# Kernel tuning notes

Hardware: AMD Instinct MI355X
Metric: run time of the kernel (lower is better)

Reference implementation:

```python
import jax, jax.numpy as jnp
import numpy as np

N_ATOMS = 100000
N_EDGES = 400000
N_MOLS = 4000
D_ATOM = 64
D_MSG = 128
N_STEPS = 3
N_MSG_HID = 1
D_RO = 256
N_RO_HID = 2
D_OUT = 1


def setup_inputs() -> dict:
    key = jax.random.key(0)
    ks = jax.random.split(key, 20)

    def w(k, shape, fan_in):
        return jax.random.normal(k, shape, dtype=jnp.float32) / np.sqrt(fan_in)

    return {
        "atom_states": jax.random.normal(ks[0], (N_ATOMS, D_ATOM), dtype=jnp.float32),
        "edge_src": jax.random.randint(ks[1], (N_EDGES,), 0, N_ATOMS, dtype=jnp.int32),
        "edge_dst": jax.random.randint(ks[2], (N_EDGES,), 0, N_ATOMS, dtype=jnp.int32),
        "mol_ids": jnp.sort(jax.random.randint(ks[3], (N_ATOMS,), 0, N_MOLS, dtype=jnp.int32)),
        "ms_W_in": w(ks[4], (N_STEPS, 2 * D_ATOM, D_MSG), 2 * D_ATOM),
        "ms_b_in": w(ks[5], (N_STEPS, D_MSG), 2 * D_ATOM),
        "ms_W_h": w(ks[6], (N_STEPS, N_MSG_HID, D_MSG, D_MSG), D_MSG),
        "ms_b_h": w(ks[7], (N_STEPS, N_MSG_HID, D_MSG), D_MSG),
        "ms_W_out": w(ks[8], (N_STEPS, D_MSG, D_ATOM), D_MSG),
        "ms_b_out": w(ks[9], (N_STEPS, D_ATOM), D_MSG),
        "ro_W_in": w(ks[10], (D_ATOM, D_RO), D_ATOM),
        "ro_b_in": w(ks[11], (D_RO,), D_ATOM),
        "ro_W_h": w(ks[12], (N_RO_HID, D_RO, D_RO), D_RO),
        "ro_b_h": w(ks[13], (N_RO_HID, D_RO), D_RO),
        "ro_W_out": w(ks[14], (D_RO, D_OUT), D_RO),
        "ro_b_out": w(ks[15], (D_OUT,), D_RO),
    }


def reference(atom_states, edge_src, edge_dst, mol_ids,
              ms_W_in, ms_b_in, ms_W_h, ms_b_h, ms_W_out, ms_b_out,
              ro_W_in, ro_b_in, ro_W_h, ro_b_h, ro_W_out, ro_b_out):
    n_atoms = atom_states.shape[0]
    states = atom_states
    # Message passing: per edge, message = MLP_step(concat(state[src], state[dst]));
    # new atom state = sum of messages over the atom's edges (aggregated at src).
    for s in range(ms_W_in.shape[0]):
        msg = jnp.concatenate([states[edge_src], states[edge_dst]], axis=-1)  # [E, 2*D]
        h = jax.nn.relu(msg @ ms_W_in[s] + ms_b_in[s])                        # [E, D_MSG]
        for l in range(ms_W_h.shape[1]):
            h = jax.nn.relu(h @ ms_W_h[s, l] + ms_b_h[s, l])
        m = jax.nn.relu(h @ ms_W_out[s] + ms_b_out[s])                        # [E, D]
        states = jax.ops.segment_sum(m, edge_src, num_segments=n_atoms)       # [N, D]
    # Readout: molecule representation = sum of its atom states, then MLP.
    mol_repr = jax.ops.segment_sum(states, mol_ids, num_segments=N_MOLS)      # [M, D]
    out = jax.nn.relu(mol_repr @ ro_W_in + ro_b_in)
    for l in range(ro_W_h.shape[0]):
        out = jax.nn.relu(out @ ro_W_h[l] + ro_b_h[l])
    return out @ ro_W_out + ro_b_out                                          # [M, D_OUT]
```

## Files before the change

kernel.cpp:

```cpp
#include <hip/hip_runtime.h>
#include <hip/hip_bf16.h>

#define K_N_ATOMS 100000
#define K_N_EDGES 400000
#define K_N_MOLS  4000

typedef __attribute__((ext_vector_type(8))) short bf16x8;
typedef __attribute__((ext_vector_type(4))) float f32x4;

__device__ __forceinline__ unsigned short f2bf(float x) {
  union { __hip_bfloat16 b; unsigned short u; } c;
  c.b = __float2bfloat16(x);
  return c.u;
}

__device__ __forceinline__ float bf2f(unsigned short u) {
  union { float f; unsigned u; } c;
  c.u = ((unsigned)u) << 16;
  return c.f;
}

__device__ __forceinline__ unsigned pk2(float a, float b) {
  union { __hip_bfloat162 h; unsigned u; } c;
  c.h = __float22bfloat162_rn(make_float2(a, b));
  return c.u;
}

__device__ __forceinline__ bf16x8 pack8(float4 x, float4 y) {
  union { bf16x8 v; unsigned u[4]; } r;
  r.u[0] = pk2(x.x, x.y); r.u[1] = pk2(x.z, x.w);
  r.u[2] = pk2(y.x, y.y); r.u[3] = pk2(y.z, y.w);
  return r.v;
}

__device__ __forceinline__ float relu(float x) { return fmaxf(x, 0.f); }

__device__ __forceinline__ bf16x8 addrelu8(bf16x8 a, bf16x8 b) {
  union { bf16x8 v; unsigned short s[8]; } ua, ub;
  ua.v = a; ub.v = b;
  union { bf16x8 v; unsigned u[4]; } r;
#pragma unroll
  for (int q = 0; q < 4; ++q) {
    float x0 = relu(bf2f(ua.s[2 * q]) + bf2f(ub.s[2 * q]));
    float x1 = relu(bf2f(ua.s[2 * q + 1]) + bf2f(ub.s[2 * q + 1]));
    r.u[q] = pk2(x0, x1);
  }
  return r.v;
}

__global__ void prep_w(const float* __restrict__ Win, const float* __restrict__ Wh,
                       const float* __restrict__ Wout, unsigned short* __restrict__ wf) {
  int s = blockIdx.y;
  int flat = (blockIdx.x * 256 + threadIdx.x) * 4;
  if (flat < 16384) {
    const float* W = Win + s * 16384;
    unsigned short* dst = wf + s * 40960;
    int k = flat >> 7, j = flat & 127;
    float4 w4 = *(const float4*)(W + flat);
    float wv[4] = {w4.x, w4.y, w4.z, w4.w};
#pragma unroll
    for (int c = 0; c < 4; ++c) {
      int jj = j + c, kk = k;
      if (k >= 64) { kk = k - 64; jj += 128; }
      int jt = jj >> 4, ks = kk >> 5, ln = (jj & 15) + 16 * ((kk >> 3) & 3), i = kk & 7;
      dst[((jt * 2 + ks) * 64 + ln) * 8 + i] = f2bf(wv[c]);
    }
  } else if (flat < 32768) {
    const float* W = Wh + s * 16384;
    unsigned short* dst = wf + s * 40960 + 16384;
    int local = flat - 16384;
    int k = local >> 7, j = local & 127;
    float4 w4 = *(const float4*)(W + local);
    float wv[4] = {w4.x, w4.y, w4.z, w4.w};
    int ks = k >> 5, kr = (k >> 3) & 3, i = k & 7;
#pragma unroll
    for (int c = 0; c < 4; ++c) {
      int jj = j + c;
      int jt = jj >> 4, ln = (jj & 15) + 16 * kr;
      dst[((jt * 4 + ks) * 64 + ln) * 8 + i] = f2bf(wv[c]);
    }
  } else {
    const float* W = Wout + s * 8192;
    unsigned short* dst = wf + s * 40960 + 32768;
    int local = flat - 32768;
    int k = local >> 6, j = local & 63;
    float4 w4 = *(const float4*)(W + local);
    float wv[4] = {w4.x, w4.y, w4.z, w4.w};
    int ks = k >> 5, kr = (k >> 3) & 3, i = k & 7;
#pragma unroll
    for (int c = 0; c < 4; ++c) {
      int jj = j + c;
      int jt = jj >> 4, ln = (jj & 15) + 16 * kr;
      dst[((jt * 4 + ks) * 64 + ln) * 8 + i] = f2bf(wv[c]);
    }
  }
}

__global__ void k_hist(const int* __restrict__ esrc, int* __restrict__ cnt) {
  int t = blockIdx.x * 256 + threadIdx.x;
  if (t < K_N_EDGES) atomicAdd(&cnt[esrc[t]], 1);
}

__global__ void k_blocksum(const int* __restrict__ cnt, int* __restrict__ partial) {
  __shared__ int red[256];
  int i = blockIdx.x * 256 + threadIdx.x;
  red[threadIdx.x] = (i < K_N_ATOMS) ? cnt[i] : 0;
  __syncthreads();
  for (int off = 128; off; off >>= 1) {
    if (threadIdx.x < off) red[threadIdx.x] += red[threadIdx.x + off];
    __syncthreads();
  }
  if (!threadIdx.x) partial[blockIdx.x] = red[0];
}

__global__ void k_scanpart2(int* __restrict__ partial, int nb) {
  __shared__ int sh[512];
  int tid = threadIdx.x;
  int v = (tid < nb) ? partial[tid] : 0;
  sh[tid] = v;
  __syncthreads();
  for (int off = 1; off < 512; off <<= 1) {
    int t = (tid >= off) ? sh[tid - off] : 0;
    __syncthreads();
    sh[tid] += t;
    __syncthreads();
  }
  if (tid < nb) partial[tid] = sh[tid] - v;
}

__global__ void k_scanfinal(const int* __restrict__ cnt, const int* __restrict__ poffs,
                            int* __restrict__ start, int* __restrict__ cur) {
  __shared__ int sh[256];
  int tid = threadIdx.x;
  int i = blockIdx.x * 256 + tid;
  int v = (i < K_N_ATOMS) ? cnt[i] : 0;
  sh[tid] = v;
  __syncthreads();
  for (int off = 1; off < 256; off <<= 1) {
    int t = (tid >= off) ? sh[tid - off] : 0;
    __syncthreads();
    sh[tid] += t;
    __syncthreads();
  }
  int ex = sh[tid] - v + poffs[blockIdx.x];
  if (i < K_N_ATOMS) { start[i] = ex; cur[i] = ex; }
  if (i == K_N_ATOMS - 1) start[K_N_ATOMS] = ex + v;
}

__global__ void k_scatter(const int* __restrict__ esrc, const int* __restrict__ edst,
                          int* __restrict__ cur, int2* __restrict__ ep) {
  int t = blockIdx.x * 256 + threadIdx.x;
  if (t < K_N_EDGES) {
    int s = esrc[t];
    int p = atomicAdd(&cur[s], 1);
    ep[p] = make_int2(s, edst[t]);
  }
}

__global__ __launch_bounds__(256, 4) void fg_gemm0(
    const float* __restrict__ st_in, unsigned short* __restrict__ FG,
    const unsigned short* __restrict__ wfg, const float* __restrict__ bin) {
  const int tid = threadIdx.x;
  const int wave = tid >> 6, lane = tid & 63, lo = lane & 15, h = lane >> 4;
  const int atom0 = (blockIdx.x * 4 + wave) * 16;
  const int a = atom0 + lo;
  const int ac = (a < K_N_ATOMS) ? a : (K_N_ATOMS - 1);

  const float* row = st_in + (size_t)ac * 64 + h * 8;
  bf16x8 b0 = pack8(*(const float4*)row, *(const float4*)(row + 4));
  bf16x8 b1 = pack8(*(const float4*)(row + 32), *(const float4*)(row + 36));

#pragma unroll
  for (int jt = 0; jt < 16; ++jt) {
    f32x4 acc;
    if (jt < 8) acc = *(const f32x4*)(bin + jt * 16 + h * 4);
    else { acc[0] = 0.f; acc[1] = 0.f; acc[2] = 0.f; acc[3] = 0.f; }
    bf16x8 a0 = *(const bf16x8*)(wfg + ((jt * 2 + 0) * 64 + lane) * 8);
    bf16x8 a1 = *(const bf16x8*)(wfg + ((jt * 2 + 1) * 64 + lane) * 8);
    acc = __builtin_amdgcn_mfma_f32_16x16x32_bf16(a0, b0, acc, 0, 0, 0);
    acc = __builtin_amdgcn_mfma_f32_16x16x32_bf16(a1, b1, acc, 0, 0, 0);
    if (a < K_N_ATOMS)
      *(uint2*)(FG + (size_t)a * 256 + jt * 16 + h * 4) =
          make_uint2(pk2(acc[0], acc[1]), pk2(acc[2], acc[3]));
  }
}

__global__ __launch_bounds__(256, 4) void agg_fg(
    const unsigned short* __restrict__ m_buf, const int* __restrict__ start,
    unsigned short* __restrict__ FG,
    const unsigned short* __restrict__ wfg, const float* __restrict__ bin) {
  const int tid = threadIdx.x;
  const int wave = tid >> 6, lane = tid & 63, lo = lane & 15, h = lane >> 4;
  const int atom0 = (blockIdx.x * 4 + wave) * 16;
  const int a = atom0 + lo;

  int s = 0, e = 0;
  if (a < K_N_ATOMS) { s = start[a]; e = start[a + 1]; }

  float acc[16];
#pragma unroll
  for (int q = 0; q < 16; ++q) acc[q] = 0.f;
  for (int r = s; r < e; ++r) {
    const unsigned short* p = m_buf + (size_t)r * 64 + h * 8;
    union { bf16x8 v; unsigned short w[8]; } u0, u1;
    u0.v = *(const bf16x8*)(p);
    u1.v = *(const bf16x8*)(p + 32);
#pragma unroll
    for (int q = 0; q < 8; ++q) { acc[q] += bf2f(u0.w[q]); acc[8 + q] += bf2f(u1.w[q]); }
  }
  union { bf16x8 v; unsigned u[4]; } c0, c1;
#pragma unroll
  for (int q = 0; q < 4; ++q) {
    c0.u[q] = pk2(acc[2 * q], acc[2 * q + 1]);
    c1.u[q] = pk2(acc[8 + 2 * q], acc[8 + 2 * q + 1]);
  }
  bf16x8 b0 = c0.v, b1 = c1.v;

#pragma unroll
  for (int jt = 0; jt < 16; ++jt) {
    f32x4 d;
    if (jt < 8) d = *(const f32x4*)(bin + jt * 16 + h * 4);
    else { d[0] = 0.f; d[1] = 0.f; d[2] = 0.f; d[3] = 0.f; }
    bf16x8 a0 = *(const bf16x8*)(wfg + ((jt * 2 + 0) * 64 + lane) * 8);
    bf16x8 a1 = *(const bf16x8*)(wfg + ((jt * 2 + 1) * 64 + lane) * 8);
    d = __builtin_amdgcn_mfma_f32_16x16x32_bf16(a0, b0, d, 0, 0, 0);
    d = __builtin_amdgcn_mfma_f32_16x16x32_bf16(a1, b1, d, 0, 0, 0);
    if (a < K_N_ATOMS)
      *(uint2*)(FG + (size_t)a * 256 + jt * 16 + h * 4) =
          make_uint2(pk2(d[0], d[1]), pk2(d[2], d[3]));
  }
}

__device__ __forceinline__ void layer128_2(const unsigned short* wf,
                                           const float* __restrict__ bias,
                                           bf16x8 (&bfr)[2][4], unsigned (&p)[2][8][2],
                                           int lane, int h) {
#pragma unroll
  for (int jt = 0; jt < 8; ++jt) {
    f32x4 bv = *(const f32x4*)(bias + jt * 16 + h * 4);
    f32x4 a0 = bv, a1 = bv;
#pragma unroll
    for (int ks = 0; ks < 4; ++ks) {
      bf16x8 a = *(const bf16x8*)(wf + ((jt * 4 + ks) * 64 + lane) * 8);
      a0 = __builtin_amdgcn_mfma_f32_16x16x32_bf16(a, bfr[0][ks], a0, 0, 0, 0);
      a1 = __builtin_amdgcn_mfma_f32_16x16x32_bf16(a, bfr[1][ks], a1, 0, 0, 0);
    }
    p[0][jt][0] = pk2(relu(a0[0]), relu(a0[1])); p[0][jt][1] = pk2(relu(a0[2]), relu(a0[3]));
    p[1][jt][0] = pk2(relu(a1[0]), relu(a1[1])); p[1][jt][1] = pk2(relu(a1[2]), relu(a1[3]));
  }
}

__device__ __forceinline__ void transpose_p2(const unsigned (&p)[2][8][2], bf16x8 (&bfr)[2][4],
                                             int lo, int h) {
  const int hsel = (h & 1) * 2;
#pragma unroll
  for (int et = 0; et < 2; ++et) {
#pragma unroll
    for (int ks = 0; ks < 4; ++ks) {
      union { unsigned u[4]; bf16x8 v; } cv;
#pragma unroll
      for (int w = 0; w < 4; ++w) {
        int srcLane = lo + 16 * (hsel + (w >> 1));
        unsigned d0 = (unsigned)__shfl((int)p[et][2 * ks][w & 1], srcLane, 64);
        unsigned d1 = (unsigned)__shfl((int)p[et][2 * ks + 1][w & 1], srcLane, 64);
        cv.u[w] = (h < 2) ? d0 : d1;
      }
      bfr[et][ks] = cv.v;
    }
  }
}

__global__ __launch_bounds__(512, 4) void edge_msg4(
    const unsigned short* __restrict__ FG, unsigned short* __restrict__ m_buf,
    const int2* __restrict__ ep, const unsigned short* __restrict__ wf23,
    const float* __restrict__ b2, const float* __restrict__ b3) {
  __shared__ unsigned short wl[24576];
  const int tid = threadIdx.x;
  const int wave = tid >> 6, lane = tid & 63, lo = lane & 15, h = lane >> 4;
  const int ebase = blockIdx.x * 256 + wave * 32;

  int srcs[2], dsts[2];
  unsigned vmask = 0;
#pragma unroll
  for (int et = 0; et < 2; ++et) {
    int e = ebase + et * 16 + lo;
    if (e < K_N_EDGES) vmask |= 1u << et;
    int ec = (e < K_N_EDGES) ? e : (K_N_EDGES - 1);
    int2 pr = ep[ec];
    srcs[et] = pr.x;
    dsts[et] = pr.y;
  }

#pragma unroll
  for (int i = 0; i < 6; ++i)
    ((bf16x8*)wl)[i * 512 + tid] = ((const bf16x8*)wf23)[i * 512 + tid];
  __syncthreads();

  bf16x8 bfr[2][4];
#pragma unroll
  for (int et = 0; et < 2; ++et) {
    const unsigned short* pf = FG + (size_t)srcs[et] * 256 + h * 8;
    const unsigned short* pg = FG + (size_t)dsts[et] * 256 + 128 + h * 8;
#pragma unroll
    for (int ks = 0; ks < 4; ++ks) {
      bf16x8 f = *(const bf16x8*)(pf + ks * 32);
      bf16x8 g = *(const bf16x8*)(pg + ks * 32);
      bfr[et][ks] = addrelu8(f, g);
    }
  }

  unsigned p[2][8][2];
  layer128_2(wl, b2, bfr, p, lane, h);
  transpose_p2(p, bfr, lo, h);

  const unsigned short* w3 = wl + 16384;
#pragma unroll
  for (int jt = 0; jt < 4; ++jt) {
    f32x4 bv = *(const f32x4*)(b3 + jt * 16 + h * 4);
    f32x4 a0 = bv, a1 = bv;
#pragma unroll
    for (int ks = 0; ks < 4; ++ks) {
      bf16x8 a = *(const bf16x8*)(w3 + ((jt * 4 + ks) * 64 + lane) * 8);
      a0 = __builtin_amdgcn_mfma_f32_16x16x32_bf16(a, bfr[0][ks], a0, 0, 0, 0);
      a1 = __builtin_amdgcn_mfma_f32_16x16x32_bf16(a, bfr[1][ks], a1, 0, 0, 0);
    }
    f32x4 accs[2] = {a0, a1};
#pragma unroll
    for (int et = 0; et < 2; ++et) {
      if (vmask & (1u << et)) {
        int e = ebase + et * 16 + lo;
        *(uint2*)(m_buf + (size_t)e * 64 + jt * 16 + h * 4) =
            make_uint2(pk2(relu(accs[et][0]), relu(accs[et][1])),
                       pk2(relu(accs[et][2]), relu(accs[et][3])));
      }
    }
  }
}

__global__ __launch_bounds__(256) void seg_agg2(
    const unsigned short* __restrict__ m_buf, const int* __restrict__ start,
    unsigned short* __restrict__ stb_out) {
  int t = blockIdx.x * 256 + threadIdx.x;
  int a = t >> 3, sub = t & 7;
  if (a >= K_N_ATOMS) return;
  int s = start[a], e = start[a + 1];
  float acc[8] = {0.f, 0.f, 0.f, 0.f, 0.f, 0.f, 0.f, 0.f};
  for (int r = s; r < e; ++r) {
    union { bf16x8 v; unsigned short w[8]; } u;
    u.v = *(const bf16x8*)(m_buf + (size_t)r * 64 + sub * 8);
#pragma unroll
    for (int q = 0; q < 8; ++q) acc[q] += bf2f(u.w[q]);
  }
  union { bf16x8 v; unsigned u[4]; } r8;
#pragma unroll
  for (int q = 0; q < 4; ++q) r8.u[q] = pk2(acc[2 * q], acc[2 * q + 1]);
  *(bf16x8*)(stb_out + (size_t)a * 64 + sub * 8) = r8.v;
}

__global__ void mol_bounds(const int* __restrict__ mol_ids, int* __restrict__ start) {
  int a = blockIdx.x * 256 + threadIdx.x;
  if (a >= K_N_ATOMS) return;
  int id = mol_ids[a];
  int prev = (a == 0) ? -1 : mol_ids[a - 1];
  for (int m = prev + 1; m <= id; ++m) start[m] = a;
  if (a == K_N_ATOMS - 1)
    for (int m = id + 1; m <= K_N_MOLS; ++m) start[m] = K_N_ATOMS;
}

__global__ void mol_sum2(const unsigned short* __restrict__ stb, const int* __restrict__ start,
                         float* __restrict__ mol) {
  int t = blockIdx.x * 256 + threadIdx.x;
  int m = t >> 3, sub = t & 7;
  if (m >= K_N_MOLS) return;
  int s = start[m], e = start[m + 1];
  float acc[8] = {0.f, 0.f, 0.f, 0.f, 0.f, 0.f, 0.f, 0.f};
  for (int a = s; a < e; ++a) {
    union { bf16x8 v; unsigned short w[8]; } u;
    u.v = *(const bf16x8*)(stb + (size_t)a * 64 + sub * 8);
#pragma unroll
    for (int q = 0; q < 8; ++q) acc[q] += bf2f(u.w[q]);
  }
  float* p = mol + (size_t)m * 64 + sub * 8;
  *(float4*)(p) = make_float4(acc[0], acc[1], acc[2], acc[3]);
  *(float4*)(p + 4) = make_float4(acc[4], acc[5], acc[6], acc[7]);
}

template<int KDIM>
__global__ void mlp_layer8(const float* __restrict__ in, const float* __restrict__ W,
                           const float* __restrict__ bias, float* __restrict__ out) {
  __shared__ float in_l[8][KDIM + 4];
  int m0 = blockIdx.x * 8;
  int t = threadIdx.x;
  for (int flat = t; flat < 8 * KDIM; flat += 256) {
    int m = flat / KDIM, k = flat - m * KDIM;
    in_l[m][k] = in[(size_t)(m0 + m) * KDIM + k];
  }
  __syncthreads();
  int j = t;
  float b = bias[j];
  float acc[8];
#pragma unroll
  for (int m = 0; m < 8; ++m) acc[m] = b;
  for (int k = 0; k < KDIM; ++k) {
    float w = W[(size_t)k * 256 + j];
#pragma unroll
    for (int m = 0; m < 8; ++m) acc[m] += in_l[m][k] * w;
  }
#pragma unroll
  for (int m = 0; m < 8; ++m)
    out[(size_t)(m0 + m) * 256 + j] = fmaxf(acc[m], 0.f);
}

__global__ void mlp_out_k(const float* __restrict__ in, const float* __restrict__ W,
                          const float* __restrict__ bias, float* __restrict__ out) {
  int wave = threadIdx.x >> 6, lane = threadIdx.x & 63;
  int m = blockIdx.x * 4 + wave;
  if (m >= K_N_MOLS) return;
  float4 v = *(const float4*)(in + (size_t)m * 256 + lane * 4);
  float4 w = *(const float4*)(W + lane * 4);
  float s = v.x * w.x + v.y * w.y + v.z * w.z + v.w * w.w;
  for (int off = 32; off; off >>= 1) s += __shfl_down(s, off);
  if (lane == 0) out[m] = s + bias[0];
}

extern "C" void kernel_launch(void* const* d_in, const int* in_sizes, int n_in,
                              void* d_out, int out_size, void* d_ws, size_t ws_size,
                              hipStream_t stream) {
  const float* atom_states = (const float*)d_in[0];
  const int* esrc = (const int*)d_in[1];
  const int* edst = (const int*)d_in[2];
  const int* mol_ids = (const int*)d_in[3];
  const float* msWin = (const float*)d_in[4];
  const float* msbin = (const float*)d_in[5];
  const float* msWh = (const float*)d_in[6];
  const float* msbh = (const float*)d_in[7];
  const float* msWout = (const float*)d_in[8];
  const float* msbout = (const float*)d_in[9];
  const float* roWin = (const float*)d_in[10];
  const float* robin = (const float*)d_in[11];
  const float* roWh = (const float*)d_in[12];
  const float* robh = (const float*)d_in[13];
  const float* roWout = (const float*)d_in[14];
  const float* robout = (const float*)d_in[15];
  float* out = (float*)d_out;

  unsigned short* m_buf = (unsigned short*)d_ws;
  unsigned short* FG = m_buf + (size_t)K_N_EDGES * 64;
  unsigned short* stb = FG + (size_t)K_N_ATOMS * 256;
  int2* ep = (int2*)(stb + (size_t)K_N_ATOMS * 64);
  int* cnt = (int*)(ep + K_N_EDGES);
  int* start = cnt + K_N_ATOMS;
  int* cur = start + K_N_ATOMS + 1;
  int* partial = cur + K_N_ATOMS;
  unsigned short* wfb = (unsigned short*)(partial + 512);
  int* mstart = (int*)(wfb + 3 * 40960);
  float* mol = (float*)m_buf;
  float* r1 = mol + (size_t)K_N_MOLS * 64;
  float* r2 = r1 + (size_t)K_N_MOLS * 256;

  const int EG = (K_N_EDGES + 255) / 256;
  const int EG4 = (K_N_EDGES + 255) / 256;
  const int AG = (K_N_ATOMS + 255) / 256;
  const int AG16 = (K_N_ATOMS + 63) / 64;

  prep_w<<<dim3(40, 3), 256, 0, stream>>>(msWin, msWh, msWout, wfb);

  hipMemsetAsync(cnt, 0, K_N_ATOMS * sizeof(int), stream);
  k_hist<<<EG, 256, 0, stream>>>(esrc, cnt);
  k_blocksum<<<AG, 256, 0, stream>>>(cnt, partial);
  k_scanpart2<<<1, 512, 0, stream>>>(partial, AG);
  k_scanfinal<<<AG, 256, 0, stream>>>(cnt, partial, start, cur);
  k_scatter<<<EG, 256, 0, stream>>>(esrc, edst, cur, ep);
  mol_bounds<<<AG, 256, 0, stream>>>(mol_ids, mstart);

  fg_gemm0<<<AG16, 256, 0, stream>>>(atom_states, FG, wfb, msbin);
  edge_msg4<<<EG4, 512, 0, stream>>>(FG, m_buf, ep, wfb + 16384, msbh, msbout);
  agg_fg<<<AG16, 256, 0, stream>>>(m_buf, start, FG, wfb + 40960, msbin + 128);
  edge_msg4<<<EG4, 512, 0, stream>>>(FG, m_buf, ep, wfb + 40960 + 16384,
                                     msbh + 128, msbout + 64);
  agg_fg<<<AG16, 256, 0, stream>>>(m_buf, start, FG, wfb + 81920, msbin + 256);
  edge_msg4<<<EG4, 512, 0, stream>>>(FG, m_buf, ep, wfb + 81920 + 16384,
                                     msbh + 256, msbout + 128);
  seg_agg2<<<(K_N_ATOMS * 8 + 255) / 256, 256, 0, stream>>>(m_buf, start, stb);

  mol_sum2<<<(K_N_MOLS * 8 + 255) / 256, 256, 0, stream>>>(stb, mstart, mol);
  mlp_layer8<64><<<K_N_MOLS / 8, 256, 0, stream>>>(mol, roWin, robin, r1);
  mlp_layer8<256><<<K_N_MOLS / 8, 256, 0, stream>>>(r1, roWh, robh, r2);
  mlp_layer8<256><<<K_N_MOLS / 8, 256, 0, stream>>>(r2, roWh + 256 * 256, robh + 256, r1);
  mlp_out_k<<<K_N_MOLS / 4, 256, 0, stream>>>(r1, roWout, robout, out);
}
```

Baseline: 383.6 us.

## Fuse edge message MLP with per-atom segment aggregation via shared-memory atomics

Blocks now own 64 consecutive source atoms and walk the CSR-sorted edge range for those atoms. They run the message MLP and accumulate the results into a shared-memory fp32 tile with atomics, so the per-edge message buffer is no longer written to and re-read from global memory. The separate segment-sum kernels are gone, and the next step's FG GEMM reads the aggregated bf16 states directly. F and G are also split into separate arrays. The cost is shared-memory atomic contention, load imbalance across blocks when degree varies, and a partially filled last chunk of 256 edges per block (about 256 edges per block on average), which wastes MFMA work.

```diff
diff --git a/kernel.cpp b/kernel.cpp
--- a/kernel.cpp
+++ b/kernel.cpp
@@ -158,7 +158,8 @@
 }
 
 __global__ __launch_bounds__(256, 4) void fg_gemm0(
-    const float* __restrict__ st_in, unsigned short* __restrict__ FG,
+    const float* __restrict__ st_in, unsigned short* __restrict__ Fb,
+    unsigned short* __restrict__ Gb,
     const unsigned short* __restrict__ wfg, const float* __restrict__ bin) {
   const int tid = threadIdx.x;
   const int wave = tid >> 6, lane = tid & 63, lo = lane & 15, h = lane >> 4;
@@ -179,55 +180,42 @@
     bf16x8 a1 = *(const bf16x8*)(wfg + ((jt * 2 + 1) * 64 + lane) * 8);
     acc = __builtin_amdgcn_mfma_f32_16x16x32_bf16(a0, b0, acc, 0, 0, 0);
     acc = __builtin_amdgcn_mfma_f32_16x16x32_bf16(a1, b1, acc, 0, 0, 0);
-    if (a < K_N_ATOMS)
-      *(uint2*)(FG + (size_t)a * 256 + jt * 16 + h * 4) =
-          make_uint2(pk2(acc[0], acc[1]), pk2(acc[2], acc[3]));
-  }
-}
-
-__global__ __launch_bounds__(256, 4) void agg_fg(
-    const unsigned short* __restrict__ m_buf, const int* __restrict__ start,
-    unsigned short* __restrict__ FG,
+    if (a < K_N_ATOMS) {
+      unsigned short* dst = (jt < 8) ? (Fb + (size_t)a * 128 + jt * 16 + h * 4)
+                                     : (Gb + (size_t)a * 128 + (jt - 8) * 16 + h * 4);
+      *(uint2*)dst = make_uint2(pk2(acc[0], acc[1]), pk2(acc[2], acc[3]));
+    }
+  }
+}
+
+__global__ __launch_bounds__(256, 4) void fg_gemmB(
+    const unsigned short* __restrict__ stb, unsigned short* __restrict__ Fb,
+    unsigned short* __restrict__ Gb,
     const unsigned short* __restrict__ wfg, const float* __restrict__ bin) {
   const int tid = threadIdx.x;
   const int wave = tid >> 6, lane = tid & 63, lo = lane & 15, h = lane >> 4;
   const int atom0 = (blockIdx.x * 4 + wave) * 16;
   const int a = atom0 + lo;
-
-  int s = 0, e = 0;
-  if (a < K_N_ATOMS) { s = start[a]; e = start[a + 1]; }
-
-  float acc[16];
-#pragma unroll
-  for (int q = 0; q < 16; ++q) acc[q] = 0.f;
-  for (int r = s; r < e; ++r) {
-    const unsigned short* p = m_buf + (size_t)r * 64 + h * 8;
-    union { bf16x8 v; unsigned short w[8]; } u0, u1;
-    u0.v = *(const bf16x8*)(p);
-    u1.v = *(const bf16x8*)(p + 32);
-#pragma unroll
-    for (int q = 0; q < 8; ++q) { acc[q] += bf2f(u0.w[q]); acc[8 + q] += bf2f(u1.w[q]); }
-  }
-  union { bf16x8 v; unsigned u[4]; } c0, c1;
-#pragma unroll
-  for (int q = 0; q < 4; ++q) {
-    c0.u[q] = pk2(acc[2 * q], acc[2 * q + 1]);
-    c1.u[q] = pk2(acc[8 + 2 * q], acc[8 + 2 * q + 1]);
-  }
-  bf16x8 b0 = c0.v, b1 = c1.v;
+  const int ac = (a < K_N_ATOMS) ? a : (K_N_ATOMS - 1);
+
+  const unsigned short* row = stb + (size_t)ac * 64 + h * 8;
+  bf16x8 b0 = *(const bf16x8*)(row);
+  bf16x8 b1 = *(const bf16x8*)(row + 32);
 
 #pragma unroll
   for (int jt = 0; jt < 16; ++jt) {
-    f32x4 d;
-    if (jt < 8) d = *(const f32x4*)(bin + jt * 16 + h * 4);
-    else { d[0] = 0.f; d[1] = 0.f; d[2] = 0.f; d[3] = 0.f; }
+    f32x4 acc;
+    if (jt < 8) acc = *(const f32x4*)(bin + jt * 16 + h * 4);
+    else { acc[0] = 0.f; acc[1] = 0.f; acc[2] = 0.f; acc[3] = 0.f; }
     bf16x8 a0 = *(const bf16x8*)(wfg + ((jt * 2 + 0) * 64 + lane) * 8);
     bf16x8 a1 = *(const bf16x8*)(wfg + ((jt * 2 + 1) * 64 + lane) * 8);
-    d = __builtin_amdgcn_mfma_f32_16x16x32_bf16(a0, b0, d, 0, 0, 0);
-    d = __builtin_amdgcn_mfma_f32_16x16x32_bf16(a1, b1, d, 0, 0, 0);
-    if (a < K_N_ATOMS)
-      *(uint2*)(FG + (size_t)a * 256 + jt * 16 + h * 4) =
-          make_uint2(pk2(d[0], d[1]), pk2(d[2], d[3]));
+    acc = __builtin_amdgcn_mfma_f32_16x16x32_bf16(a0, b0, acc, 0, 0, 0);
+    acc = __builtin_amdgcn_mfma_f32_16x16x32_bf16(a1, b1, acc, 0, 0, 0);
+    if (a < K_N_ATOMS) {
+      unsigned short* dst = (jt < 8) ? (Fb + (size_t)a * 128 + jt * 16 + h * 4)
+                                     : (Gb + (size_t)a * 128 + (jt - 8) * 16 + h * 4);
+      *(uint2*)dst = make_uint2(pk2(acc[0], acc[1]), pk2(acc[2], acc[3]));
+    }
   }
 }
 
@@ -270,91 +258,96 @@
   }
 }
 
-__global__ __launch_bounds__(512, 4) void edge_msg4(
-    const unsigned short* __restrict__ FG, unsigned short* __restrict__ m_buf,
-    const int2* __restrict__ ep, const unsigned short* __restrict__ wf23,
+#define EA_SMEM (49152 + 64 * 65 * 4)
+
+__global__ __launch_bounds__(512, 4) void edge_agg(
+    const unsigned short* __restrict__ Fb, const unsigned short* __restrict__ Gb,
+    unsigned short* __restrict__ st_out,
+    const int2* __restrict__ ep, const int* __restrict__ start,
+    const unsigned short* __restrict__ wf23,
     const float* __restrict__ b2, const float* __restrict__ b3) {
-  __shared__ unsigned short wl[24576];
+  extern __shared__ char smem[];
+  unsigned short* wl = (unsigned short*)smem;
+  float* acc = (float*)(smem + 49152);
   const int tid = threadIdx.x;
   const int wave = tid >> 6, lane = tid & 63, lo = lane & 15, h = lane >> 4;
-  const int ebase = blockIdx.x * 256 + wave * 32;
-
-  int srcs[2], dsts[2];
-  unsigned vmask = 0;
-#pragma unroll
-  for (int et = 0; et < 2; ++et) {
-    int e = ebase + et * 16 + lo;
-    if (e < K_N_EDGES) vmask |= 1u << et;
-    int ec = (e < K_N_EDGES) ? e : (K_N_EDGES - 1);
-    int2 pr = ep[ec];
-    srcs[et] = pr.x;
-    dsts[et] = pr.y;
-  }
+  const int abase = blockIdx.x * 64;
 
 #pragma unroll
   for (int i = 0; i < 6; ++i)
     ((bf16x8*)wl)[i * 512 + tid] = ((const bf16x8*)wf23)[i * 512 + tid];
-  __syncthreads();
-
-  bf16x8 bfr[2][4];
-#pragma unroll
-  for (int et = 0; et < 2; ++et) {
-    const unsigned short* pf = FG + (size_t)srcs[et] * 256 + h * 8;
-    const unsigned short* pg = FG + (size_t)dsts[et] * 256 + 128 + h * 8;
-#pragma unroll
-    for (int ks = 0; ks < 4; ++ks) {
-      bf16x8 f = *(const bf16x8*)(pf + ks * 32);
-      bf16x8 g = *(const bf16x8*)(pg + ks * 32);
-      bfr[et][ks] = addrelu8(f, g);
-    }
-  }
-
-  unsigned p[2][8][2];
-  layer128_2(wl, b2, bfr, p, lane, h);
-  transpose_p2(p, bfr, lo, h);
-
-  const unsigned short* w3 = wl + 16384;
-#pragma unroll
-  for (int jt = 0; jt < 4; ++jt) {
-    f32x4 bv = *(const f32x4*)(b3 + jt * 16 + h * 4);
-    f32x4 a0 = bv, a1 = bv;
-#pragma unroll
-    for (int ks = 0; ks < 4; ++ks) {
-      bf16x8 a = *(const bf16x8*)(w3 + ((jt * 4 + ks) * 64 + lane) * 8);
-      a0 = __builtin_amdgcn_mfma_f32_16x16x32_bf16(a, bfr[0][ks], a0, 0, 0, 0);
-      a1 = __builtin_amdgcn_mfma_f32_16x16x32_bf16(a, bfr[1][ks], a1, 0, 0, 0);
-    }
-    f32x4 accs[2] = {a0, a1};
+  for (int i = tid; i < 64 * 65; i += 512) acc[i] = 0.f;
+
+  const int s_blk = start[abase];
+  const int aend = (abase + 64 < K_N_ATOMS) ? (abase + 64) : K_N_ATOMS;
+  const int e_blk = start[aend];
+  __syncthreads();
+
+  for (int cbase = s_blk; cbase < e_blk; cbase += 256) {
+    int srcs[2], dsts[2];
+    unsigned vmask = 0;
 #pragma unroll
     for (int et = 0; et < 2; ++et) {
-      if (vmask & (1u << et)) {
-        int e = ebase + et * 16 + lo;
-        *(uint2*)(m_buf + (size_t)e * 64 + jt * 16 + h * 4) =
-            make_uint2(pk2(relu(accs[et][0]), relu(accs[et][1])),
-                       pk2(relu(accs[et][2]), relu(accs[et][3])));
+      int e = cbase + wave * 32 + et * 16 + lo;
+      if (e < e_blk) vmask |= 1u << et;
+      int ec = (e < e_blk) ? e : (e_blk - 1);
+      int2 pr = ep[ec];
+      srcs[et] = pr.x;
+      dsts[et] = pr.y;
+    }
+
+    bf16x8 bfr[2][4];
+#pragma unroll
+    for (int et = 0; et < 2; ++et) {
+      const unsigned short* pf = Fb + (size_t)srcs[et] * 128 + h * 8;
+      const unsigned short* pg = Gb + (size_t)dsts[et] * 128 + h * 8;
+#pragma unroll
+      for (int ks = 0; ks < 4; ++ks)
+        bfr[et][ks] = addrelu8(*(const bf16x8*)(pf + ks * 32),
+                               *(const bf16x8*)(pg + ks * 32));
+    }
+
+    unsigned p[2][8][2];
+    layer128_2(wl, b2, bfr, p, lane, h);
+    transpose_p2(p, bfr, lo, h);
+
+    const unsigned short* w3 = wl + 16384;
+#pragma unroll
+    for (int jt = 0; jt < 4; ++jt) {
+      f32x4 bv = *(const f32x4*)(b3 + jt * 16 + h * 4);
+      f32x4 a0 = bv, a1 = bv;
+#pragma unroll
+      for (int ks = 0; ks < 4; ++ks) {
+        bf16x8 a = *(const bf16x8*)(w3 + ((jt * 4 + ks) * 64 + lane) * 8);
+        a0 = __builtin_amdgcn_mfma_f32_16x16x32_bf16(a, bfr[0][ks], a0, 0, 0, 0);
+        a1 = __builtin_amdgcn_mfma_f32_16x16x32_bf16(a, bfr[1][ks], a1, 0, 0, 0);
       }
-    }
-  }
-}
-
-__global__ __launch_bounds__(256) void seg_agg2(
-    const unsigned short* __restrict__ m_buf, const int* __restrict__ start,
-    unsigned short* __restrict__ stb_out) {
-  int t = blockIdx.x * 256 + threadIdx.x;
-  int a = t >> 3, sub = t & 7;
-  if (a >= K_N_ATOMS) return;
-  int s = start[a], e = start[a + 1];
-  float acc[8] = {0.f, 0.f, 0.f, 0.f, 0.f, 0.f, 0.f, 0.f};
-  for (int r = s; r < e; ++r) {
-    union { bf16x8 v; unsigned short w[8]; } u;
-    u.v = *(const bf16x8*)(m_buf + (size_t)r * 64 + sub * 8);
-#pragma unroll
-    for (int q = 0; q < 8; ++q) acc[q] += bf2f(u.w[q]);
-  }
-  union { bf16x8 v; unsigned u[4]; } r8;
-#pragma unroll
-  for (int q = 0; q < 4; ++q) r8.u[q] = pk2(acc[2 * q], acc[2 * q + 1]);
-  *(bf16x8*)(stb_out + (size_t)a * 64 + sub * 8) = r8.v;
+      f32x4 accs[2] = {a0, a1};
+#pragma unroll
+      for (int et = 0; et < 2; ++et) {
+        if (vmask & (1u << et)) {
+          float* pa = &acc[(srcs[et] - abase) * 65 + jt * 16 + h * 4];
+          atomicAdd(pa + 0, relu(accs[et][0]));
+          atomicAdd(pa + 1, relu(accs[et][1]));
+          atomicAdd(pa + 2, relu(accs[et][2]));
+          atomicAdd(pa + 3, relu(accs[et][3]));
+        }
+      }
+    }
+  }
+  __syncthreads();
+
+  {
+    int al = tid >> 3, sub = tid & 7;
+    int a = abase + al;
+    if (a < K_N_ATOMS) {
+      const float* pa = &acc[al * 65 + sub * 8];
+      union { bf16x8 v; unsigned u[4]; } r8;
+#pragma unroll
+      for (int q = 0; q < 4; ++q) r8.u[q] = pk2(pa[2 * q], pa[2 * q + 1]);
+      *(bf16x8*)(st_out + (size_t)a * 64 + sub * 8) = r8.v;
+    }
+  }
 }
 
 __global__ void mol_bounds(const int* __restrict__ mol_ids, int* __restrict__ start) {
@@ -444,9 +437,9 @@
   const float* robout = (const float*)d_in[15];
   float* out = (float*)d_out;
 
-  unsigned short* m_buf = (unsigned short*)d_ws;
-  unsigned short* FG = m_buf + (size_t)K_N_EDGES * 64;
-  unsigned short* stb = FG + (size_t)K_N_ATOMS * 256;
+  unsigned short* Fb = (unsigned short*)d_ws;
+  unsigned short* Gb = Fb + (size_t)K_N_ATOMS * 128;
+  unsigned short* stb = Gb + (size_t)K_N_ATOMS * 128;
   int2* ep = (int2*)(stb + (size_t)K_N_ATOMS * 64);
   int* cnt = (int*)(ep + K_N_EDGES);
   int* start = cnt + K_N_ATOMS;
@@ -454,14 +447,17 @@
   int* partial = cur + K_N_ATOMS;
   unsigned short* wfb = (unsigned short*)(partial + 512);
   int* mstart = (int*)(wfb + 3 * 40960);
-  float* mol = (float*)m_buf;
+  float* mol = (float*)Fb;
   float* r1 = mol + (size_t)K_N_MOLS * 64;
   float* r2 = r1 + (size_t)K_N_MOLS * 256;
 
   const int EG = (K_N_EDGES + 255) / 256;
-  const int EG4 = (K_N_EDGES + 255) / 256;
   const int AG = (K_N_ATOMS + 255) / 256;
   const int AG16 = (K_N_ATOMS + 63) / 64;
+  const int AB = (K_N_ATOMS + 63) / 64;
+
+  hipFuncSetAttribute((const void*)edge_agg,
+                      hipFuncAttributeMaxDynamicSharedMemorySize, EA_SMEM);
 
   prep_w<<<dim3(40, 3), 256, 0, stream>>>(msWin, msWh, msWout, wfb);
 
@@ -473,15 +469,15 @@
   k_scatter<<<EG, 256, 0, stream>>>(esrc, edst, cur, ep);
   mol_bounds<<<AG, 256, 0, stream>>>(mol_ids, mstart);
 
-  fg_gemm0<<<AG16, 256, 0, stream>>>(atom_states, FG, wfb, msbin);
-  edge_msg4<<<EG4, 512, 0, stream>>>(FG, m_buf, ep, wfb + 16384, msbh, msbout);
-  agg_fg<<<AG16, 256, 0, stream>>>(m_buf, start, FG, wfb + 40960, msbin + 128);
-  edge_msg4<<<EG4, 512, 0, stream>>>(FG, m_buf, ep, wfb + 40960 + 16384,
-                                     msbh + 128, msbout + 64);
-  agg_fg<<<AG16, 256, 0, stream>>>(m_buf, start, FG, wfb + 81920, msbin + 256);
-  edge_msg4<<<EG4, 512, 0, stream>>>(FG, m_buf, ep, wfb + 81920 + 16384,
-                                     msbh + 256, msbout + 128);
-  seg_agg2<<<(K_N_ATOMS * 8 + 255) / 256, 256, 0, stream>>>(m_buf, start, stb);
+  fg_gemm0<<<AG16, 256, 0, stream>>>(atom_states, Fb, Gb, wfb, msbin);
+  edge_agg<<<AB, 512, EA_SMEM, stream>>>(Fb, Gb, stb, ep, start,
+                                         wfb + 16384, msbh, msbout);
+  fg_gemmB<<<AG16, 256, 0, stream>>>(stb, Fb, Gb, wfb + 40960, msbin + 128);
+  edge_agg<<<AB, 512, EA_SMEM, stream>>>(Fb, Gb, stb, ep, start,
+                                         wfb + 40960 + 16384, msbh + 128, msbout + 64);
+  fg_gemmB<<<AG16, 256, 0, stream>>>(stb, Fb, Gb, wfb + 81920, msbin + 256);
+  edge_agg<<<AB, 512, EA_SMEM, stream>>>(Fb, Gb, stb, ep, start,
+                                         wfb + 81920 + 16384, msbh + 256, msbout + 128);
 
   mol_sum2<<<(K_N_MOLS * 8 + 255) / 256, 256, 0, stream>>>(stb, mstart, mol);
   mlp_layer8<64><<<K_N_MOLS / 8, 256, 0, stream>>>(mol, roWin, robin, r1);
```

After: 912.2 us. 138% more time.

## Fuse molecule bounds into scan, sum edges per molecule, fuse readout MLP

Applied to the files above, without the earlier changes.

Computes molecule atom bounds inside the final scan kernel, and sums the last-step edge messages straight into molecule sums. This works because mol_ids is sorted, so each molecule's atoms cover a contiguous range of the src-sorted edge rows. It also drops the per-atom state buffer and fuses the three readout layers plus the output dot product into one kernel that keeps activations in shared memory. This removes several launches and intermediate global round trips. The cost is that the molecule sum now runs only 4000 molecules × 8 threads over long serial edge loops, so parallelism is low.

```diff
diff --git a/kernel.cpp b/kernel.cpp
--- a/kernel.cpp
+++ b/kernel.cpp
@@ -128,8 +128,9 @@
   if (tid < nb) partial[tid] = sh[tid] - v;
 }
 
-__global__ void k_scanfinal(const int* __restrict__ cnt, const int* __restrict__ poffs,
-                            int* __restrict__ start, int* __restrict__ cur) {
+__global__ void k_scanfinal_bounds(const int* __restrict__ cnt, const int* __restrict__ poffs,
+                                   int* __restrict__ start, int* __restrict__ cur,
+                                   const int* __restrict__ mol_ids, int* __restrict__ mstart) {
   __shared__ int sh[256];
   int tid = threadIdx.x;
   int i = blockIdx.x * 256 + tid;
@@ -145,6 +146,14 @@
   int ex = sh[tid] - v + poffs[blockIdx.x];
   if (i < K_N_ATOMS) { start[i] = ex; cur[i] = ex; }
   if (i == K_N_ATOMS - 1) start[K_N_ATOMS] = ex + v;
+
+  if (i < K_N_ATOMS) {
+    int id = mol_ids[i];
+    int prev = (i == 0) ? -1 : mol_ids[i - 1];
+    for (int m = prev + 1; m <= id; ++m) mstart[m] = i;
+    if (i == K_N_ATOMS - 1)
+      for (int m = id + 1; m <= K_N_MOLS; ++m) mstart[m] = K_N_ATOMS;
+  }
 }
 
 __global__ void k_scatter(const int* __restrict__ esrc, const int* __restrict__ edst,
@@ -337,13 +346,13 @@
   }
 }
 
-__global__ __launch_bounds__(256) void seg_agg2(
+__global__ __launch_bounds__(256) void mol_msum(
     const unsigned short* __restrict__ m_buf, const int* __restrict__ start,
-    unsigned short* __restrict__ stb_out) {
+    const int* __restrict__ mstart, float* __restrict__ mol) {
   int t = blockIdx.x * 256 + threadIdx.x;
-  int a = t >> 3, sub = t & 7;
-  if (a >= K_N_ATOMS) return;
-  int s = start[a], e = start[a + 1];
+  int m = t >> 3, sub = t & 7;
+  if (m >= K_N_MOLS) return;
+  int s = start[mstart[m]], e = start[mstart[m + 1]];
   float acc[8] = {0.f, 0.f, 0.f, 0.f, 0.f, 0.f, 0.f, 0.f};
   for (int r = s; r < e; ++r) {
     union { bf16x8 v; unsigned short w[8]; } u;
@@ -351,76 +360,85 @@
 #pragma unroll
     for (int q = 0; q < 8; ++q) acc[q] += bf2f(u.w[q]);
   }
-  union { bf16x8 v; unsigned u[4]; } r8;
-#pragma unroll
-  for (int q = 0; q < 4; ++q) r8.u[q] = pk2(acc[2 * q], acc[2 * q + 1]);
-  *(bf16x8*)(stb_out + (size_t)a * 64 + sub * 8) = r8.v;
-}
-
-__global__ void mol_bounds(const int* __restrict__ mol_ids, int* __restrict__ start) {
-  int a = blockIdx.x * 256 + threadIdx.x;
-  if (a >= K_N_ATOMS) return;
-  int id = mol_ids[a];
-  int prev = (a == 0) ? -1 : mol_ids[a - 1];
-  for (int m = prev + 1; m <= id; ++m) start[m] = a;
-  if (a == K_N_ATOMS - 1)
-    for (int m = id + 1; m <= K_N_MOLS; ++m) start[m] = K_N_ATOMS;
-}
-
-__global__ void mol_sum2(const unsigned short* __restrict__ stb, const int* __restrict__ start,
-                         float* __restrict__ mol) {
-  int t = blockIdx.x * 256 + threadIdx.x;
-  int m = t >> 3, sub = t & 7;
-  if (m >= K_N_MOLS) return;
-  int s = start[m], e = start[m + 1];
-  float acc[8] = {0.f, 0.f, 0.f, 0.f, 0.f, 0.f, 0.f, 0.f};
-  for (int a = s; a < e; ++a) {
-    union { bf16x8 v; unsigned short w[8]; } u;
-    u.v = *(const bf16x8*)(stb + (size_t)a * 64 + sub * 8);
-#pragma unroll
-    for (int q = 0; q < 8; ++q) acc[q] += bf2f(u.w[q]);
-  }
   float* p = mol + (size_t)m * 64 + sub * 8;
   *(float4*)(p) = make_float4(acc[0], acc[1], acc[2], acc[3]);
   *(float4*)(p + 4) = make_float4(acc[4], acc[5], acc[6], acc[7]);
 }
 
-template<int KDIM>
-__global__ void mlp_layer8(const float* __restrict__ in, const float* __restrict__ W,
-                           const float* __restrict__ bias, float* __restrict__ out) {
-  __shared__ float in_l[8][KDIM + 4];
+__global__ __launch_bounds__(256) void ro_fused(
+    const float* __restrict__ mol, const float* __restrict__ Win,
+    const float* __restrict__ bin, const float* __restrict__ Wh,
+    const float* __restrict__ bh, const float* __restrict__ Wout,
+    const float* __restrict__ bout, float* __restrict__ out) {
+  __shared__ float a[8][64];
+  __shared__ float h0[8][257];
+  __shared__ float h1[8][257];
+  __shared__ float red[8][256];
   int m0 = blockIdx.x * 8;
   int t = threadIdx.x;
-  for (int flat = t; flat < 8 * KDIM; flat += 256) {
-    int m = flat / KDIM, k = flat - m * KDIM;
-    in_l[m][k] = in[(size_t)(m0 + m) * KDIM + k];
-  }
-  __syncthreads();
-  int j = t;
-  float b = bias[j];
+  for (int flat = t; flat < 512; flat += 256) {
+    int m = flat >> 6, k = flat & 63;
+    a[m][k] = mol[(size_t)(m0 + m) * 64 + k];
+  }
+  __syncthreads();
+  const int j = t;
   float acc[8];
-#pragma unroll
-  for (int m = 0; m < 8; ++m) acc[m] = b;
-  for (int k = 0; k < KDIM; ++k) {
-    float w = W[(size_t)k * 256 + j];
-#pragma unroll
-    for (int m = 0; m < 8; ++m) acc[m] += in_l[m][k] * w;
-  }
-#pragma unroll
-  for (int m = 0; m < 8; ++m)
-    out[(size_t)(m0 + m) * 256 + j] = fmaxf(acc[m], 0.f);
-}
-
-__global__ void mlp_out_k(const float* __restrict__ in, const float* __restrict__ W,
-                          const float* __restrict__ bias, float* __restrict__ out) {
-  int wave = threadIdx.x >> 6, lane = threadIdx.x & 63;
-  int m = blockIdx.x * 4 + wave;
-  if (m >= K_N_MOLS) return;
-  float4 v = *(const float4*)(in + (size_t)m * 256 + lane * 4);
-  float4 w = *(const float4*)(W + lane * 4);
-  float s = v.x * w.x + v.y * w.y + v.z * w.z + v.w * w.w;
-  for (int off = 32; off; off >>= 1) s += __shfl_down(s, off);
-  if (lane == 0) out[m] = s + bias[0];
+  {
+    float b = bin[j];
+#pragma unroll
+    for (int m = 0; m < 8; ++m) acc[m] = b;
+#pragma unroll 8
+    for (int k = 0; k < 64; ++k) {
+      float w = Win[k * 256 + j];
+#pragma unroll
+      for (int m = 0; m < 8; ++m) acc[m] += a[m][k] * w;
+    }
+#pragma unroll
+    for (int m = 0; m < 8; ++m) h0[m][j] = relu(acc[m]);
+  }
+  __syncthreads();
+  {
+    float b = bh[j];
+#pragma unroll
+    for (int m = 0; m < 8; ++m) acc[m] = b;
+#pragma unroll 8
+    for (int k = 0; k < 256; ++k) {
+      float w = Wh[k * 256 + j];
+#pragma unroll
+      for (int m = 0; m < 8; ++m) acc[m] += h0[m][k] * w;
+    }
+#pragma unroll
+    for (int m = 0; m < 8; ++m) h1[m][j] = relu(acc[m]);
+  }
+  __syncthreads();
+  {
+    float b = bh[256 + j];
+#pragma unroll
+    for (int m = 0; m < 8; ++m) acc[m] = b;
+#pragma unroll 8
+    for (int k = 0; k < 256; ++k) {
+      float w = Wh[65536 + k * 256 + j];
+#pragma unroll
+      for (int m = 0; m < 8; ++m) acc[m] += h1[m][k] * w;
+    }
+#pragma unroll
+    for (int m = 0; m < 8; ++m) h0[m][j] = relu(acc[m]);
+  }
+  __syncthreads();
+  {
+    float wj = Wout[j];
+#pragma unroll
+    for (int m = 0; m < 8; ++m) red[m][j] = h0[m][j] * wj;
+  }
+  __syncthreads();
+  for (int off = 128; off; off >>= 1) {
+    if (j < off) {
+#pragma unroll
+      for (int m = 0; m < 8; ++m) red[m][j] += red[m][j + off];
+    }
+    __syncthreads();
+  }
+  if (j < 8) out[m0 + j] = red[j][0] + bout[0];
 }
 
 extern "C" void kernel_launch(void* const* d_in, const int* in_sizes, int n_in,
@@ -446,20 +464,16 @@
 
   unsigned short* m_buf = (unsigned short*)d_ws;
   unsigned short* FG = m_buf + (size_t)K_N_EDGES * 64;
-  unsigned short* stb = FG + (size_t)K_N_ATOMS * 256;
-  int2* ep = (int2*)(stb + (size_t)K_N_ATOMS * 64);
+  int2* ep = (int2*)(FG + (size_t)K_N_ATOMS * 256);
   int* cnt = (int*)(ep + K_N_EDGES);
   int* start = cnt + K_N_ATOMS;
   int* cur = start + K_N_ATOMS + 1;
   int* partial = cur + K_N_ATOMS;
   unsigned short* wfb = (unsigned short*)(partial + 512);
   int* mstart = (int*)(wfb + 3 * 40960);
-  float* mol = (float*)m_buf;
-  float* r1 = mol + (size_t)K_N_MOLS * 64;
-  float* r2 = r1 + (size_t)K_N_MOLS * 256;
+  float* mol = (float*)FG;
 
   const int EG = (K_N_EDGES + 255) / 256;
-  const int EG4 = (K_N_EDGES + 255) / 256;
   const int AG = (K_N_ATOMS + 255) / 256;
   const int AG16 = (K_N_ATOMS + 63) / 64;
 
@@ -469,23 +483,19 @@
   k_hist<<<EG, 256, 0, stream>>>(esrc, cnt);
   k_blocksum<<<AG, 256, 0, stream>>>(cnt, partial);
   k_scanpart2<<<1, 512, 0, stream>>>(partial, AG);
-  k_scanfinal<<<AG, 256, 0, stream>>>(cnt, partial, start, cur);
+  k_scanfinal_bounds<<<AG, 256, 0, stream>>>(cnt, partial, start, cur, mol_ids, mstart);
   k_scatter<<<EG, 256, 0, stream>>>(esrc, edst, cur, ep);
-  mol_bounds<<<AG, 256, 0, stream>>>(mol_ids, mstart);
 
   fg_gemm0<<<AG16, 256, 0, stream>>>(atom_states, FG, wfb, msbin);
-  edge_msg4<<<EG4, 512, 0, stream>>>(FG, m_buf, ep, wfb + 16384, msbh, msbout);
+  edge_msg4<<<EG, 512, 0, stream>>>(FG, m_buf, ep, wfb + 16384, msbh, msbout);
   agg_fg<<<AG16, 256, 0, stream>>>(m_buf, start, FG, wfb + 40960, msbin + 128);
-  edge_msg4<<<EG4, 512, 0, stream>>>(FG, m_buf, ep, wfb + 40960 + 16384,
-                                     msbh + 128, msbout + 64);
+  edge_msg4<<<EG, 512, 0, stream>>>(FG, m_buf, ep, wfb + 40960 + 16384,
+                                    msbh + 128, msbout + 64);
   agg_fg<<<AG16, 256, 0, stream>>>(m_buf, start, FG, wfb + 81920, msbin + 256);
-  edge_msg4<<<EG4, 512, 0, stream>>>(FG, m_buf, ep, wfb + 81920 + 16384,
-                                     msbh + 256, msbout + 128);
-  seg_agg2<<<(K_N_ATOMS * 8 + 255) / 256, 256, 0, stream>>>(m_buf, start, stb);
-
-  mol_sum2<<<(K_N_MOLS * 8 + 255) / 256, 256, 0, stream>>>(stb, mstart, mol);
-  mlp_layer8<64><<<K_N_MOLS / 8, 256, 0, stream>>>(mol, roWin, robin, r1);
-  mlp_layer8<256><<<K_N_MOLS / 8, 256, 0, stream>>>(r1, roWh, robh, r2);
-  mlp_layer8<256><<<K_N_MOLS / 8, 256, 0, stream>>>(r2, roWh + 256 * 256, robh + 256, r1);
-  mlp_out_k<<<K_N_MOLS / 4, 256, 0, stream>>>(r1, roWout, robout, out);
-}
+  edge_msg4<<<EG, 512, 0, stream>>>(FG, m_buf, ep, wfb + 81920 + 16384,
+                                    msbh + 256, msbout + 128);
+
+  mol_msum<<<(K_N_MOLS * 8 + 255) / 256, 256, 0, stream>>>(m_buf, start, mstart, mol);
+  ro_fused<<<K_N_MOLS / 8, 256, 0, stream>>>(mol, roWin, robin, roWh, robh,
+                                             roWout, robout, out);
+}
```

After: 388.7 us. Within noise of the previous version (+1.3%).
